# Performance work log

Measured on AMD Instinct MI355X. Metric: run time of the kernel, lower is better.

The kernel has to match this reference:

```python
import jax, jax.numpy as jnp
import numpy as np

B, V, D, H = 8192, 5, 1792, 14
HD = D // H  # head dim = 128
NEG = jnp.float32(-1e30)  # stand-in for -inf in the adjacency mask


def setup_inputs() -> dict:
    key = jax.random.key(0)
    ks = jax.random.split(key, 5)
    vertices = jax.random.normal(ks[0], (B, V, D), dtype=jnp.float32)
    adjacency = jax.random.randint(ks[1], (V, V), 0, 2, dtype=jnp.int32)
    # ensure no all-masked row (self connection), matching a valid pentachoron graph
    adjacency = adjacency.at[jnp.arange(V), jnp.arange(V)].set(1)
    scale = 1.0 / np.sqrt(D)
    in_proj_w = jax.random.normal(ks[2], (3 * D, D), dtype=jnp.float32) * scale
    in_proj_b = jnp.zeros((3 * D,), dtype=jnp.float32)
    out_proj_w = jax.random.normal(ks[3], (D, D), dtype=jnp.float32) * scale
    out_proj_b = jnp.zeros((D,), dtype=jnp.float32)
    return {"vertices": vertices, "adjacency": adjacency,
            "in_proj_w": in_proj_w, "in_proj_b": in_proj_b,
            "out_proj_w": out_proj_w, "out_proj_b": out_proj_b}


def reference(vertices, adjacency, in_proj_w, in_proj_b, out_proj_w, out_proj_b):
    # Fused equivalent of looping MultiheadAttention over the 5 vertices:
    # query i attends over all 5 vertices, masked by adjacency row i.
    qkv = jnp.einsum('bvd,ed->bve', vertices, in_proj_w) + in_proj_b  # [B,V,3D]
    q, k, v = jnp.split(qkv, 3, axis=-1)
    # [B,H,V,HD]
    q = q.reshape(B, V, H, HD).transpose(0, 2, 1, 3)
    k = k.reshape(B, V, H, HD).transpose(0, 2, 1, 3)
    v = v.reshape(B, V, H, HD).transpose(0, 2, 1, 3)
    scores = jnp.einsum('bhqd,bhkd->bhqk', q, k) / jnp.float32(np.sqrt(HD))
    mask = jnp.where(adjacency == 0, NEG, jnp.float32(0.0))  # [V,V]
    scores = scores + mask[None, None, :, :]
    attn = jax.nn.softmax(scores, axis=-1)
    out = jnp.einsum('bhqk,bhkd->bhqd', attn, v)  # [B,H,V,HD]
    out = out.transpose(0, 2, 1, 3).reshape(B, V, D)
    return jnp.einsum('bvd,ed->bve', out, out_proj_w) + out_proj_b
```

## Files before the change

kernel.cpp:

```cpp
#include <hip/hip_runtime.h>
#include <hip/hip_bf16.h>

#define Bsz   8192
#define Vn    5
#define Dm    1792
#define Hn    14
#define HDm   128
#define Mrows (Bsz * Vn)
#define N1    (3 * Dm)
#define Kd    Dm

typedef float f32x4 __attribute__((ext_vector_type(4)));
typedef short bf16x8 __attribute__((ext_vector_type(8)));

__device__ __forceinline__ ushort f2bf(float f) {
    unsigned u = __float_as_uint(f);
    u += 0x7fffu + ((u >> 16) & 1u);
    return (ushort)(u >> 16);
}
__device__ __forceinline__ float bf2f(ushort h) {
    return __uint_as_float(((unsigned)h) << 16);
}

#define AS1(p) ((const __attribute__((address_space(1))) void*)(p))
#define AS3(p) ((__attribute__((address_space(3))) void*)(p))

__global__ void cvt_kernel(const float* __restrict__ in, ushort* __restrict__ out, int n4) {
    int i = blockIdx.x * blockDim.x + threadIdx.x;
    int stride = gridDim.x * blockDim.x;
    for (int idx = i; idx < n4; idx += stride) {
        float4 v = reinterpret_cast<const float4*>(in)[idx];
        ushort4 o;
        o.x = f2bf(v.x); o.y = f2bf(v.y); o.z = f2bf(v.z); o.w = f2bf(v.w);
        reinterpret_cast<ushort4*>(out)[idx] = o;
    }
}

template<bool OUT_BF16>
__global__ __launch_bounds__(512, 2) void gemm8p(
    const ushort* __restrict__ A,
    const ushort* __restrict__ Bw,
    const float* __restrict__ bias,
    void* __restrict__ Cout,
    int M, int N, int K)
{
    __shared__ __align__(16) char smem[131072];

    const int nTN = N >> 8;
    int bid = blockIdx.x;
    int cpx = gridDim.x >> 3;
    int swz = (bid & 7) * cpx + (bid >> 3);
    int bm = swz / nTN, bn = swz % nTN;

    int t = threadIdx.x;
    int lane = t & 63, w = t >> 6;
    int wrow = (w >> 2) * 128;
    int wcol = (w & 3) * 64;
    int fr = lane & 15, fq = lane >> 4;
    int slotC = ((fq ^ (lane & 3)) << 4);
    int aOff = (wrow + fr) * 64 + slotC;
    int bOff = 32768 + (wcol + fr) * 64 + slotC;

    size_t K2 = (size_t)K * 2;
    size_t rowSkip = (size_t)128 * K2;
    int rowL = t >> 2;
    int slotSw = (((t & 3) ^ ((t >> 2) & 3)) << 4);
    const char* aSrc = (const char*)A + (size_t)(bm * 256 + rowL) * K2 + slotSw;
    const char* bSrc = (const char*)Bw + (size_t)(bn * 256 + rowL) * K2 + slotSw;

    f32x4 acc[8][4] = {};
    bf16x8 af[4], bf[4];

#define STAGE(SRC, UOFF, KT, KH) { \
    const char* _s = (SRC) + (size_t)(KT) * 128 + (KH) * 64; \
    __builtin_amdgcn_global_load_lds(AS1(_s), AS3(&smem[(UOFF) + t * 16]), 16, 0, 0); \
    __builtin_amdgcn_global_load_lds(AS1(_s + rowSkip), AS3(&smem[(UOFF) + 8192 + t * 16]), 16, 0, 0); }

#define DSA4(BUF, KS, M0) { \
    af[0] = *(const bf16x8*)&smem[(BUF)*65536 + (KS)*16384 + ((M0)+0)*1024 + aOff]; \
    af[1] = *(const bf16x8*)&smem[(BUF)*65536 + (KS)*16384 + ((M0)+1)*1024 + aOff]; \
    af[2] = *(const bf16x8*)&smem[(BUF)*65536 + (KS)*16384 + ((M0)+2)*1024 + aOff]; \
    af[3] = *(const bf16x8*)&smem[(BUF)*65536 + (KS)*16384 + ((M0)+3)*1024 + aOff]; }

#define DSB4(BUF, KS) { \
    bf[0] = *(const bf16x8*)&smem[(BUF)*65536 + (KS)*16384 + 0*1024 + bOff]; \
    bf[1] = *(const bf16x8*)&smem[(BUF)*65536 + (KS)*16384 + 1*1024 + bOff]; \
    bf[2] = *(const bf16x8*)&smem[(BUF)*65536 + (KS)*16384 + 2*1024 + bOff]; \
    bf[3] = *(const bf16x8*)&smem[(BUF)*65536 + (KS)*16384 + 3*1024 + bOff]; }

#define MFMAQ(M0) { \
    __builtin_amdgcn_s_setprio(1); \
    _Pragma("unroll") \
    for (int mi = 0; mi < 4; ++mi) { \
      _Pragma("unroll") \
      for (int ni = 0; ni < 4; ++ni) \
        acc[(M0)+mi][ni] = __builtin_amdgcn_mfma_f32_16x16x32_bf16(af[mi], bf[ni], acc[(M0)+mi][ni], 0, 0, 0); \
    } \
    __builtin_amdgcn_s_setprio(0); }

#define BAR __builtin_amdgcn_s_barrier()
#define VM8 { asm volatile("s_waitcnt vmcnt(8)" ::: "memory"); __builtin_amdgcn_sched_barrier(0); }

    STAGE(aSrc, 0,      0, 0);
    STAGE(bSrc, 32768,  0, 0);
    STAGE(aSrc, 16384,  0, 1);
    STAGE(bSrc, 49152,  0, 1);
    STAGE(aSrc, 65536,  1, 0);
    STAGE(bSrc, 98304,  1, 0);
    VM8;
    BAR;

    const int NIT = K / 128;
    #pragma unroll 1
    for (int it = 0; it < NIT; ++it) {
        int kt1 = 2 * it + 1;
        bool more = (it < NIT - 1);
        int kt2 = 2 * it + 2, kt3 = 2 * it + 3;

        DSA4(0, 0, 0); DSB4(0, 0);
        STAGE(aSrc, 81920, kt1, 1);
        BAR; MFMAQ(0); BAR;
        DSA4(0, 0, 4);
        STAGE(bSrc, 114688, kt1, 1);
        BAR; MFMAQ(4); VM8; BAR;
        DSA4(0, 1, 0); DSB4(0, 1);
        if (more) STAGE(aSrc, 0, kt2, 0);
        BAR; MFMAQ(0); BAR;
        DSA4(0, 1, 4);
        if (more) STAGE(bSrc, 32768, kt2, 0);
        BAR; MFMAQ(4); VM8; BAR;
        DSA4(1, 0, 0); DSB4(1, 0);
        if (more) STAGE(aSrc, 16384, kt2, 1);
        BAR; MFMAQ(0); BAR;
        DSA4(1, 0, 4);
        if (more) STAGE(bSrc, 49152, kt2, 1);
        BAR; MFMAQ(4); VM8; BAR;
        DSA4(1, 1, 0); DSB4(1, 1);
        if (more) STAGE(aSrc, 65536, kt3, 0);
        BAR; MFMAQ(0); BAR;
        DSA4(1, 1, 4);
        if (more) STAGE(bSrc, 98304, kt3, 0);
        BAR; MFMAQ(4); VM8; BAR;
    }

#undef STAGE
#undef DSA4
#undef DSB4
#undef MFMAQ
#undef BAR
#undef VM8

    float*  Cf = (float*)Cout;
    ushort* Cb = (ushort*)Cout;
    #pragma unroll
    for (int mi = 0; mi < 8; ++mi) {
        int row0 = bm * 256 + wrow + mi * 16 + fq * 4;
        #pragma unroll
        for (int ni = 0; ni < 4; ++ni) {
            int col = bn * 256 + wcol + ni * 16 + fr;
            float bv = bias[col];
            #pragma unroll
            for (int rr = 0; rr < 4; ++rr) {
                float val = acc[mi][ni][rr] + bv;
                size_t off = (size_t)(row0 + rr) * N + col;
                if (OUT_BF16) Cb[off] = f2bf(val);
                else          Cf[off] = val;
            }
        }
    }
}

__global__ __launch_bounds__(256) void attn_kernel(
    const ushort* __restrict__ qkv,
    const int* __restrict__ adj,
    ushort* __restrict__ outp)
{
    int gw = blockIdx.x * 4 + (threadIdx.x >> 6);
    int lane = threadIdx.x & 63;
    int b = gw / Hn;
    int h = gw - b * Hn;

    const ushort* base = qkv + (size_t)b * 5 * N1 + h * HDm + 2 * lane;
    float q[5][2], k[5][2], v[5][2];
    #pragma unroll
    for (int i = 0; i < 5; ++i) {
        ushort2 qq = *reinterpret_cast<const ushort2*>(base + (size_t)i * N1);
        ushort2 kk = *reinterpret_cast<const ushort2*>(base + (size_t)i * N1 + Dm);
        ushort2 vv = *reinterpret_cast<const ushort2*>(base + (size_t)i * N1 + 2 * Dm);
        q[i][0] = bf2f(qq.x); q[i][1] = bf2f(qq.y);
        k[i][0] = bf2f(kk.x); k[i][1] = bf2f(kk.y);
        v[i][0] = bf2f(vv.x); v[i][1] = bf2f(vv.y);
    }

    float s[5][5];
    #pragma unroll
    for (int i = 0; i < 5; ++i)
        #pragma unroll
        for (int j = 0; j < 5; ++j) {
            float p = q[i][0] * k[j][0] + q[i][1] * k[j][1];
            #pragma unroll
            for (int off = 32; off > 0; off >>= 1)
                p += __shfl_xor(p, off);
            s[i][j] = p;
        }

    const float scale = 0.08838834764831845f;
    float aw[5][5];
    #pragma unroll
    for (int i = 0; i < 5; ++i) {
        float sv[5];
        float mx = -3.0e38f;
        #pragma unroll
        for (int j = 0; j < 5; ++j) {
            float val = s[i][j] * scale + (adj[i * 5 + j] == 0 ? -1e30f : 0.0f);
            sv[j] = val;
            mx = fmaxf(mx, val);
        }
        float denom = 0.0f;
        #pragma unroll
        for (int j = 0; j < 5; ++j) { sv[j] = __expf(sv[j] - mx); denom += sv[j]; }
        float rd = 1.0f / denom;
        #pragma unroll
        for (int j = 0; j < 5; ++j) aw[i][j] = sv[j] * rd;
    }

    ushort* ob = outp + (size_t)b * 5 * Dm + h * HDm + 2 * lane;
    #pragma unroll
    for (int i = 0; i < 5; ++i) {
        float o0 = 0.0f, o1 = 0.0f;
        #pragma unroll
        for (int j = 0; j < 5; ++j) { o0 += aw[i][j] * v[j][0]; o1 += aw[i][j] * v[j][1]; }
        ushort2 ov; ov.x = f2bf(o0); ov.y = f2bf(o1);
        *reinterpret_cast<ushort2*>(ob + (size_t)i * Dm) = ov;
    }
}

extern "C" void kernel_launch(void* const* d_in, const int* in_sizes, int n_in,
                              void* d_out, int out_size, void* d_ws, size_t ws_size,
                              hipStream_t stream) {
    const float* vertices  = (const float*)d_in[0];
    const int*   adjacency = (const int*)  d_in[1];
    const float* w1        = (const float*)d_in[2];
    const float* b1        = (const float*)d_in[3];
    const float* w2        = (const float*)d_in[4];
    const float* b2        = (const float*)d_in[5];
    float* out = (float*)d_out;

    char* ws = (char*)d_ws;
    const size_t vertBytes = (size_t)Mrows * Kd * 2;
    const size_t qkvBytes  = (size_t)Mrows * N1 * 2;
    const size_t w1Bytes   = (size_t)N1 * Kd * 2;
    const size_t w2Bytes   = (size_t)Dm * Dm * 2;
    const size_t needed    = vertBytes + qkvBytes + w1Bytes + w2Bytes;
    if (ws_size < needed) return;

    ushort* vert_bf = (ushort*)ws;
    ushort* qkv_bf  = (ushort*)(ws + vertBytes);
    ushort* w1_bf   = (ushort*)(ws + vertBytes + qkvBytes);
    ushort* w2_bf   = (ushort*)(ws + vertBytes + qkvBytes + w1Bytes);

    cvt_kernel<<<2048, 256, 0, stream>>>(vertices, vert_bf, Mrows * Kd / 4);
    cvt_kernel<<<512,  256, 0, stream>>>(w1, w1_bf, N1 * Kd / 4);
    cvt_kernel<<<256,  256, 0, stream>>>(w2, w2_bf, Dm * Dm / 4);

    gemm8p<true><<<(Mrows / 256) * (N1 / 256), 512, 0, stream>>>(
        vert_bf, w1_bf, b1, qkv_bf, Mrows, N1, Kd);

    attn_kernel<<<Bsz * Hn / 4, 256, 0, stream>>>(qkv_bf, adjacency, vert_bf);

    gemm8p<false><<<(Mrows / 256) * (Dm / 256), 512, 0, stream>>>(
        vert_bf, w2_bf, b2, out, Mrows, Dm, Kd);
}
```

Measured before the change: 1.378 ms.

## Double-buffer LDS fragment registers and change LDS swizzle in GEMM main loop

```diff
diff --git a/kernel.cpp b/kernel.cpp
--- a/kernel.cpp
+++ b/kernel.cpp
@@ -57,49 +57,49 @@
     int wrow = (w >> 2) * 128;
     int wcol = (w & 3) * 64;
     int fr = lane & 15, fq = lane >> 4;
-    int slotC = ((fq ^ (lane & 3)) << 4);
+    int slotC = ((fq ^ ((fr >> 1) & 3)) << 4);
     int aOff = (wrow + fr) * 64 + slotC;
     int bOff = 32768 + (wcol + fr) * 64 + slotC;
 
     size_t K2 = (size_t)K * 2;
     size_t rowSkip = (size_t)128 * K2;
     int rowL = t >> 2;
-    int slotSw = (((t & 3) ^ ((t >> 2) & 3)) << 4);
+    int slotSw = (((t & 3) ^ ((t >> 3) & 3)) << 4);
     const char* aSrc = (const char*)A + (size_t)(bm * 256 + rowL) * K2 + slotSw;
     const char* bSrc = (const char*)Bw + (size_t)(bn * 256 + rowL) * K2 + slotSw;
 
     f32x4 acc[8][4] = {};
-    bf16x8 af[4], bf[4];
+    bf16x8 af0[4], af1[4], bf0[4], bf1[4];
 
 #define STAGE(SRC, UOFF, KT, KH) { \
     const char* _s = (SRC) + (size_t)(KT) * 128 + (KH) * 64; \
     __builtin_amdgcn_global_load_lds(AS1(_s), AS3(&smem[(UOFF) + t * 16]), 16, 0, 0); \
     __builtin_amdgcn_global_load_lds(AS1(_s + rowSkip), AS3(&smem[(UOFF) + 8192 + t * 16]), 16, 0, 0); }
 
-#define DSA4(BUF, KS, M0) { \
-    af[0] = *(const bf16x8*)&smem[(BUF)*65536 + (KS)*16384 + ((M0)+0)*1024 + aOff]; \
-    af[1] = *(const bf16x8*)&smem[(BUF)*65536 + (KS)*16384 + ((M0)+1)*1024 + aOff]; \
-    af[2] = *(const bf16x8*)&smem[(BUF)*65536 + (KS)*16384 + ((M0)+2)*1024 + aOff]; \
-    af[3] = *(const bf16x8*)&smem[(BUF)*65536 + (KS)*16384 + ((M0)+3)*1024 + aOff]; }
-
-#define DSB4(BUF, KS) { \
-    bf[0] = *(const bf16x8*)&smem[(BUF)*65536 + (KS)*16384 + 0*1024 + bOff]; \
-    bf[1] = *(const bf16x8*)&smem[(BUF)*65536 + (KS)*16384 + 1*1024 + bOff]; \
-    bf[2] = *(const bf16x8*)&smem[(BUF)*65536 + (KS)*16384 + 2*1024 + bOff]; \
-    bf[3] = *(const bf16x8*)&smem[(BUF)*65536 + (KS)*16384 + 3*1024 + bOff]; }
-
-#define MFMAQ(M0) { \
+#define RDA(DST, BUF, KS, M0) { \
+    DST[0] = *(const bf16x8*)&smem[(BUF)*65536 + (KS)*16384 + ((M0)+0)*1024 + aOff]; \
+    DST[1] = *(const bf16x8*)&smem[(BUF)*65536 + (KS)*16384 + ((M0)+1)*1024 + aOff]; \
+    DST[2] = *(const bf16x8*)&smem[(BUF)*65536 + (KS)*16384 + ((M0)+2)*1024 + aOff]; \
+    DST[3] = *(const bf16x8*)&smem[(BUF)*65536 + (KS)*16384 + ((M0)+3)*1024 + aOff]; }
+
+#define RDB(DST, BUF, KS) { \
+    DST[0] = *(const bf16x8*)&smem[(BUF)*65536 + (KS)*16384 + 0*1024 + bOff]; \
+    DST[1] = *(const bf16x8*)&smem[(BUF)*65536 + (KS)*16384 + 1*1024 + bOff]; \
+    DST[2] = *(const bf16x8*)&smem[(BUF)*65536 + (KS)*16384 + 2*1024 + bOff]; \
+    DST[3] = *(const bf16x8*)&smem[(BUF)*65536 + (KS)*16384 + 3*1024 + bOff]; }
+
+#define MFMAQ(AF, BF, M0) { \
     __builtin_amdgcn_s_setprio(1); \
     _Pragma("unroll") \
     for (int mi = 0; mi < 4; ++mi) { \
       _Pragma("unroll") \
       for (int ni = 0; ni < 4; ++ni) \
-        acc[(M0)+mi][ni] = __builtin_amdgcn_mfma_f32_16x16x32_bf16(af[mi], bf[ni], acc[(M0)+mi][ni], 0, 0, 0); \
+        acc[(M0)+mi][ni] = __builtin_amdgcn_mfma_f32_16x16x32_bf16(AF[mi], BF[ni], acc[(M0)+mi][ni], 0, 0, 0); \
     } \
     __builtin_amdgcn_s_setprio(0); }
 
 #define BAR __builtin_amdgcn_s_barrier()
-#define VM8 { asm volatile("s_waitcnt vmcnt(8)" ::: "memory"); __builtin_amdgcn_sched_barrier(0); }
+#define VMC(N) { asm volatile("s_waitcnt vmcnt(" #N ")" ::: "memory"); __builtin_amdgcn_sched_barrier(0); }
 
     STAGE(aSrc, 0,      0, 0);
     STAGE(bSrc, 32768,  0, 0);
@@ -107,48 +107,56 @@
     STAGE(bSrc, 49152,  0, 1);
     STAGE(aSrc, 65536,  1, 0);
     STAGE(bSrc, 98304,  1, 0);
-    VM8;
+    VMC(8);
     BAR;
+    RDA(af0, 0, 0, 0); RDB(bf0, 0, 0);
 
     const int NIT = K / 128;
     #pragma unroll 1
-    for (int it = 0; it < NIT; ++it) {
-        int kt1 = 2 * it + 1;
-        bool more = (it < NIT - 1);
-        int kt2 = 2 * it + 2, kt3 = 2 * it + 3;
-
-        DSA4(0, 0, 0); DSB4(0, 0);
-        STAGE(aSrc, 81920, kt1, 1);
-        BAR; MFMAQ(0); BAR;
-        DSA4(0, 0, 4);
-        STAGE(bSrc, 114688, kt1, 1);
-        BAR; MFMAQ(4); VM8; BAR;
-        DSA4(0, 1, 0); DSB4(0, 1);
-        if (more) STAGE(aSrc, 0, kt2, 0);
-        BAR; MFMAQ(0); BAR;
-        DSA4(0, 1, 4);
-        if (more) STAGE(bSrc, 32768, kt2, 0);
-        BAR; MFMAQ(4); VM8; BAR;
-        DSA4(1, 0, 0); DSB4(1, 0);
-        if (more) STAGE(aSrc, 16384, kt2, 1);
-        BAR; MFMAQ(0); BAR;
-        DSA4(1, 0, 4);
-        if (more) STAGE(bSrc, 49152, kt2, 1);
-        BAR; MFMAQ(4); VM8; BAR;
-        DSA4(1, 1, 0); DSB4(1, 1);
-        if (more) STAGE(aSrc, 65536, kt3, 0);
-        BAR; MFMAQ(0); BAR;
-        DSA4(1, 1, 4);
-        if (more) STAGE(bSrc, 98304, kt3, 0);
-        BAR; MFMAQ(4); VM8; BAR;
+    for (int it = 0; it < NIT - 1; ++it) {
+        int kt1 = 2 * it + 1, kt2 = 2 * it + 2, kt3 = 2 * it + 3;
+        RDA(af1, 0, 0, 4);                 STAGE(aSrc, 81920, kt1, 1);
+        BAR; MFMAQ(af0, bf0, 0); VMC(6); BAR;
+        RDA(af0, 0, 1, 0); RDB(bf1, 0, 1); STAGE(bSrc, 114688, kt1, 1);
+        BAR; MFMAQ(af1, bf0, 4); BAR;
+        RDA(af1, 0, 1, 4);                 STAGE(aSrc, 0, kt2, 0);
+        BAR; MFMAQ(af0, bf1, 0); VMC(6); BAR;
+        RDA(af0, 1, 0, 0); RDB(bf0, 1, 0); STAGE(bSrc, 32768, kt2, 0);
+        BAR; MFMAQ(af1, bf1, 4); BAR;
+        RDA(af1, 1, 0, 4);                 STAGE(aSrc, 16384, kt2, 1);
+        BAR; MFMAQ(af0, bf0, 0); VMC(6); BAR;
+        RDA(af0, 1, 1, 0); RDB(bf1, 1, 1); STAGE(bSrc, 49152, kt2, 1);
+        BAR; MFMAQ(af1, bf0, 4); BAR;
+        RDA(af1, 1, 1, 4);                 STAGE(aSrc, 65536, kt3, 0);
+        BAR; MFMAQ(af0, bf1, 0); VMC(6); BAR;
+        RDA(af0, 0, 0, 0); RDB(bf0, 0, 0); STAGE(bSrc, 98304, kt3, 0);
+        BAR; MFMAQ(af1, bf1, 4); BAR;
+    }
+    {
+        int kt1 = 2 * NIT - 1;
+        RDA(af1, 0, 0, 4);                 STAGE(aSrc, 81920, kt1, 1);
+        BAR; MFMAQ(af0, bf0, 0); VMC(6); BAR;
+        RDA(af0, 0, 1, 0); RDB(bf1, 0, 1); STAGE(bSrc, 114688, kt1, 1);
+        BAR; MFMAQ(af1, bf0, 4); BAR;
+        RDA(af1, 0, 1, 4);
+        BAR; MFMAQ(af0, bf1, 0); VMC(4); BAR;
+        RDA(af0, 1, 0, 0); RDB(bf0, 1, 0);
+        BAR; MFMAQ(af1, bf1, 4); BAR;
+        RDA(af1, 1, 0, 4);
+        BAR; MFMAQ(af0, bf0, 0); VMC(0); BAR;
+        RDA(af0, 1, 1, 0); RDB(bf1, 1, 1);
+        BAR; MFMAQ(af1, bf0, 4); BAR;
+        RDA(af1, 1, 1, 4);
+        BAR; MFMAQ(af0, bf1, 0); BAR;
+        MFMAQ(af1, bf1, 4);
     }
 
 #undef STAGE
-#undef DSA4
-#undef DSB4
+#undef RDA
+#undef RDB
 #undef MFMAQ
 #undef BAR
-#undef VM8
+#undef VMC
 
     float*  Cf = (float*)Cout;
     ushort* Cb = (ushort*)Cout;
```

Result: faster. 1.328 ms (-3.6%).
